# Kernel tuning notes

Hardware: AMD Instinct MI355X
Metric: run time of the kernel (lower is better)

The kernel has to match this reference:

```python
import jax, jax.numpy as jnp
import numpy as np
from jax import lax

GRID_W, GRID_H = 4, 4
N_NODES = GRID_W * GRID_H  # 16
N_NEIGH = 8
N_CLS = 10
BN_EPS = 1e-5


def _neighbors(i, w, h, mode=8):
    # exact port of Brain.neighbors (ordering matters for the concat)
    size = w * h
    out = []
    if i - w >= 0:
        out.append(i - w)
    if i % w != 0:
        out.append(i - 1)
    if (i + 1) % w != 0:
        out.append(i + 1)
    if i + w < size:
        out.append(i + w)
    if mode == 8:
        if i - w - 1 >= 0 and i % w != 0:
            out.append(i - w - 1)
        if i - w + 1 >= 0 and (i + 1) % w != 0:
            out.append(i - w + 1)
        if i + w - 1 < size and i % w != 0:
            out.append(i + w - 1)
        if i + w + 1 < size and (i + 1) % w != 0:
            out.append(i + w + 1)
    return out


def _neighbor_table():
    idx = np.full((N_NODES, N_NEIGH), 0, dtype=np.int32)
    mask = np.zeros((N_NODES, N_NEIGH), dtype=np.float32)
    for i in range(N_NODES):
        n = _neighbors(i, GRID_W, GRID_H, 8)
        idx[i, :len(n)] = np.array(n, dtype=np.int32)
        mask[i, :len(n)] = 1.0
    return jnp.asarray(idx), jnp.asarray(mask)


def _conv(x, w, b):
    y = lax.conv_general_dilated(x, w, (1, 1), 'SAME',
                                 dimension_numbers=('NCHW', 'OIHW', 'NCHW'))
    return y + b[None, :, None, None]


def _bn_train(x, g, b):
    # BatchNorm2d in training mode (module default): batch statistics
    mean = jnp.mean(x, axis=(0, 2, 3), keepdims=True)
    var = jnp.var(x, axis=(0, 2, 3), keepdims=True)
    xn = (x - mean) * lax.rsqrt(var + BN_EPS)
    return xn * g[None, :, None, None] + b[None, :, None, None]


def _maxpool(x):
    # MaxPool2d(kernel=3, stride=2, padding=1)
    return lax.reduce_window(x, -jnp.inf, lax.max,
                             (1, 1, 3, 3), (1, 1, 2, 2),
                             ((0, 0), (0, 0), (1, 1), (1, 1)))


def setup_inputs() -> dict:
    key = jax.random.key(0)
    ks = jax.random.split(key, 24)
    B = 128
    f32 = jnp.float32

    def rn(k, shape, scale):
        return jax.random.normal(k, shape, dtype=f32) * scale

    inp = {
        'x': rn(ks[0], (B, 3, 64, 64), 1.0),
        'cw1': rn(ks[1], (64, 3, 3, 3), 0.1), 'cb1': jnp.zeros((64,), f32),
        'bn1_g': jnp.ones((64,), f32), 'bn1_b': jnp.zeros((64,), f32),
        'cw2': rn(ks[2], (128, 64, 3, 3), 0.05), 'cb2': jnp.zeros((128,), f32),
        'bn2_g': jnp.ones((128,), f32), 'bn2_b': jnp.zeros((128,), f32),
        'cw3': rn(ks[3], (256, 128, 3, 3), 0.03), 'cb3': jnp.zeros((256,), f32),
        'cw4': rn(ks[4], (256, 256, 3, 3), 0.02), 'cb4': jnp.zeros((256,), f32),
        'cw5': rn(ks[5], (512, 256, 3, 3), 0.02), 'cb5': jnp.zeros((512,), f32),
        'cw6': rn(ks[6], (512, 512, 3, 3), 0.015), 'cb6': jnp.zeros((512,), f32),
        'cw7': rn(ks[7], (512, 512, 3, 3), 0.015), 'cb7': jnp.zeros((512,), f32),
        'W1': rn(ks[8], (N_NODES, 592, 600), 0.04), 'b1': jnp.zeros((N_NODES, 600), f32),
        'W2': rn(ks[9], (N_NODES, 600, N_CLS), 0.04), 'b2': jnp.zeros((N_NODES, N_CLS), f32),
    }
    return inp


def _backbone(x, cw1, cb1, bn1_g, bn1_b, cw2, cb2, bn2_g, bn2_b,
              cw3, cb3, cw4, cb4, cw5, cb5, cw6, cb6, cw7, cb7):
    h = _maxpool(jax.nn.relu(_bn_train(_conv(x, cw1, cb1), bn1_g, bn1_b)))
    h = _maxpool(jax.nn.relu(_bn_train(_conv(h, cw2, cb2), bn2_g, bn2_b)))
    h = jax.nn.relu(_conv(h, cw3, cb3))
    h = _maxpool(jax.nn.relu(_conv(h, cw4, cb4)))
    h = jax.nn.relu(_conv(h, cw5, cb5))
    h = _maxpool(jax.nn.relu(_conv(h, cw6, cb6)))
    h = jax.nn.relu(_conv(h, cw7, cb7))
    return h  # [B, 512, 4, 4]


def _colons(X, W1, b1, W2, b2):
    # X: [16, B, 592] -> softmax probs [16, B, 10]; per-node MLP
    h = jnp.tanh(jnp.einsum('nbi,nio->nbo', X, W1) + b1[:, None, :])
    logits = jnp.einsum('nbh,nho->nbo', h, W2) + b2[:, None, :]
    return jax.nn.softmax(logits, axis=-1)


def reference(x, cw1, cb1, bn1_g, bn1_b, cw2, cb2, bn2_g, bn2_b,
              cw3, cb3, cw4, cb4, cw5, cb5, cw6, cb6, cw7, cb7,
              W1, b1, W2, b2):
    B = x.shape[0]
    conv = _backbone(x, cw1, cb1, bn1_g, bn1_b, cw2, cb2, bn2_g, bn2_b,
                     cw3, cb3, cw4, cb4, cw5, cb5, cw6, cb6, cw7, cb7)
    conv = conv.reshape(B, 512, N_NODES)           # torch.flatten(conv, 2)
    feats = jnp.transpose(conv, (2, 0, 1))         # [16, B, 512]

    # first pass: neighbor slots are all-zero p1..p8
    zeros80 = jnp.zeros((N_NODES, B, N_NEIGH * N_CLS), dtype=x.dtype)
    preds1 = _colons(jnp.concatenate([zeros80, feats], axis=-1), W1, b1, W2, b2)

    # second pass: gather neighbor predictions (zero-padded to 8 slots)
    idx, mask = _neighbor_table()                  # [16,8] int, [16,8] float
    gathered = preds1[idx]                         # [16, 8, B, 10]
    gathered = gathered * mask[:, :, None, None]
    neigh = jnp.transpose(gathered, (0, 2, 1, 3)).reshape(N_NODES, B, N_NEIGH * N_CLS)
    preds2 = _colons(jnp.concatenate([neigh, feats], axis=-1), W1, b1, W2, b2)  # [16, B, 10]

    sum_preds = jnp.mean(preds2, axis=0)           # [B, 10]
    squared_sum_preds = sum_preds * sum_preds
    return squared_sum_preds, preds2
```

## Files before the change

### kernel.cpp

```cpp
#include <hip/hip_runtime.h>
#include <math.h>


#define BN_EPS 1e-5f

typedef _Float16 f16x8 __attribute__((ext_vector_type(8)));
typedef _Float16 f16x4 __attribute__((ext_vector_type(4)));
typedef float    f32x4v __attribute__((ext_vector_type(4)));

constexpr int ilog2c(int x) { return x <= 1 ? 0 : 1 + ilog2c(x >> 1); }

__device__ __forceinline__ void lds_barrier() {
    asm volatile("s_waitcnt lgkmcnt(0)\n\ts_barrier" ::: "memory");
}

__global__ __launch_bounds__(256)
void wsplit_kernel(const float* __restrict__ w, _Float16* __restrict__ o, int COCI)
{
    const int t = blockIdx.x * 256 + threadIdx.x;
    if (t >= COCI) return;
#pragma unroll
    for (int ph = 0; ph < 9; ++ph)
        o[ph * COCI + t] = (_Float16)w[t * 9 + ph];
}

__global__ void wsplit1_kernel(const float* __restrict__ w, _Float16* __restrict__ o)
{
    const int co = threadIdx.x;
#pragma unroll
    for (int k = 0; k < 32; ++k)
        o[co * 32 + k] = (k < 27) ? (_Float16)w[co * 27 + k] : (_Float16)0.f;
}

__global__ __launch_bounds__(256)
void w1t_kernel(const float* __restrict__ W1, _Float16* __restrict__ Tf,
                _Float16* __restrict__ Tn)
{
    __shared__ float T[64][65];
    const int n  = blockIdx.z;
    const int o0 = blockIdx.y * 64;
    const int k0 = blockIdx.x * 64;
    const int tid = threadIdx.x;
    const int c  = tid & 63;
    const int r4 = tid >> 6;
    const float* Wn = W1 + (size_t)n * 592 * 600;
#pragma unroll
    for (int rep = 0; rep < 16; ++rep) {
        const int kr = rep * 4 + r4;
        const int k = k0 + kr, o = o0 + c;
        float v = 0.f;
        if (k < 592 && o < 600) v = Wn[k * 600 + o];
        T[kr][c] = v;
    }
    __syncthreads();
#pragma unroll
    for (int rep = 0; rep < 16; ++rep) {
        const int orr = rep * 4 + r4;
        const int o = o0 + orr;
        const int k = k0 + c;
        const float v = T[c][orr];
        if (k >= 80 && k < 592)
            Tf[((size_t)(n * 640 + o)) * 512 + (k - 80)] = (_Float16)v;
        if (k < 96)
            Tn[((size_t)(n * 640 + o)) * 96 + k] = (k < 80) ? (_Float16)v : (_Float16)0.f;
    }
}

__global__ void b1pad_kernel(const float* __restrict__ b1, float* __restrict__ b1p)
{
    const int t = blockIdx.x * 256 + threadIdx.x;
    if (t >= 16 * 640) return;
    const int n = t / 640, o = t - n * 640;
    b1p[t] = (o < 600) ? b1[n * 600 + o] : 0.f;
}

__global__ __launch_bounds__(256)
void conv1_mfma_kernel(const float* __restrict__ in, const _Float16* __restrict__ w32,
                       _Float16* __restrict__ out, int B)
{
    __shared__ __align__(16) _Float16 As[64 * 32];
    __shared__ __align__(16) _Float16 Bs[128 * 32];

    const int tid  = threadIdx.x;
    const int pix0 = blockIdx.x * 128;
    const int bn   = tid & 127;
    const int bh   = tid >> 7;
    const int gp   = pix0 + bn;
    const int pb   = gp >> 12;
    const int sp   = gp & 4095;
    const int py   = sp >> 6;
    const int px   = sp & 63;
    const float* inb = in + (size_t)pb * 3 * 4096;

    _Float16 vals[16];
    if (bh == 0) {
#pragma unroll
        for (int u = 0; u < 16; ++u) {
            const int k = u;
            const int ci = k / 9, r = k - ci * 9, ky = r / 3, kx = r - ky * 3;
            const int iy = py + ky - 1, ix = px + kx - 1;
            float v = 0.f;
            if ((unsigned)iy < 64u && (unsigned)ix < 64u)
                v = inb[ci * 4096 + iy * 64 + ix];
            vals[u] = (_Float16)v;
        }
    } else {
#pragma unroll
        for (int u = 0; u < 16; ++u) {
            const int k = 16 + u;
            float v = 0.f;
            if (k < 27) {
                const int ci = k / 9, r = k - ci * 9, ky = r / 3, kx = r - ky * 3;
                const int iy = py + ky - 1, ix = px + kx - 1;
                if ((unsigned)iy < 64u && (unsigned)ix < 64u)
                    v = inb[ci * 4096 + iy * 64 + ix];
            }
            vals[u] = (_Float16)v;
        }
    }
    f16x8 b0, b1;
#pragma unroll
    for (int j = 0; j < 8; ++j) { b0[j] = vals[j]; b1[j] = vals[8 + j]; }
    *(f16x8*)&Bs[bn * 32 + (((2 * bh    ) ^ (bn & 3)) << 3)] = b0;
    *(f16x8*)&Bs[bn * 32 + (((2 * bh + 1) ^ (bn & 3)) << 3)] = b1;

    if (tid < 128) {
        const int arow = tid >> 1, ah = tid & 1;
        const f16x8 a0 = *(const f16x8*)(w32 + arow * 32 + ah * 16);
        const f16x8 a1 = *(const f16x8*)(w32 + arow * 32 + ah * 16 + 8);
        *(f16x8*)&As[arow * 32 + (((2 * ah    ) ^ (arow & 3)) << 3)] = a0;
        *(f16x8*)&As[arow * 32 + (((2 * ah + 1) ^ (arow & 3)) << 3)] = a1;
    }
    __syncthreads();

    const int lane = tid & 63, wv = tid >> 6;
    const int q = lane >> 4, lm = lane & 15;
    const int swz = (q ^ (lm & 3)) << 3;

    f16x8 af[4], bf[2];
#pragma unroll
    for (int ti = 0; ti < 4; ++ti)
        af[ti] = *(const f16x8*)&As[(ti * 16 + lm) * 32 + swz];
#pragma unroll
    for (int tj = 0; tj < 2; ++tj)
        bf[tj] = *(const f16x8*)&Bs[(wv * 32 + tj * 16 + lm) * 32 + swz];

    f32x4v acc[4][2];
#pragma unroll
    for (int ti = 0; ti < 4; ++ti)
#pragma unroll
        for (int tj = 0; tj < 2; ++tj)
            acc[ti][tj] = __builtin_amdgcn_mfma_f32_16x16x32_f16(
                af[ti], bf[tj], (f32x4v)0.f, 0, 0, 0);

#pragma unroll
    for (int tj = 0; tj < 2; ++tj) {
        const int gpix = pix0 + wv * 32 + tj * 16 + lm;
#pragma unroll
        for (int ti = 0; ti < 4; ++ti) {
            const int cob = ti * 16 + q * 4;
            f16x4 h4;
#pragma unroll
            for (int r = 0; r < 4; ++r) h4[r] = (_Float16)acc[ti][tj][r];
            *(f16x4*)&out[(size_t)gpix * 64 + cob] = h4;
        }
    }
}

template <int CI, int CO, int H, int W, int KSPLIT, int EPI>
__global__ __launch_bounds__(256)
void conv_pl_kernel(const _Float16* __restrict__ in, const _Float16* __restrict__ w9,
                    const float* __restrict__ bias, _Float16* __restrict__ out,
                    float* __restrict__ part, const _Float16* __restrict__ zbuf, int B)
{
    constexpr int HW   = H * W;
    constexpr int lgHW = ilog2c(HW);
    constexpr int lgW  = ilog2c(W);

    __shared__ __align__(16) _Float16 As[2][128 * 32];

    const int tid  = threadIdx.x;
    const int pix0 = blockIdx.x * 128;
    const int co0  = blockIdx.y * 128;

    const int lane = tid & 63, wv = tid >> 6;
    const int wm = (wv & 1) * 64, wn = (wv >> 1) * 64;
    const int q = lane >> 4, lm = lane & 15;
    const int swz = (q ^ (lm & 3)) << 3;

    const int arow = tid >> 1, ah = tid & 1;
    const int aw0 = ((2 * ah    ) ^ (arow & 3)) << 3;
    const int aw1 = ((2 * ah + 1) ^ (arow & 3)) << 3;
    const _Float16* abase = w9 + ((size_t)(co0 + arow)) * CI + ah * 16;

    int pbq[4], pyq[4], pxq[4];
#pragma unroll
    for (int tj = 0; tj < 4; ++tj) {
        const int gp = pix0 + wn + tj * 16 + lm;
        pbq[tj] = gp >> lgHW;
        const int sp = gp & (HW - 1);
        pyq[tj] = sp >> lgW;
        pxq[tj] = sp & (W - 1);
    }

    constexpr int CS_TOT = CI / 32;
    constexpr int CS_PER = CS_TOT / KSPLIT;
    constexpr int NIT    = 9 * CS_PER;
    const int cs0 = (KSPLIT > 1) ? blockIdx.z * CS_PER : 0;

    const _Float16* bp[4];
    auto setB = [&](int phx) {
        const int dy = phx / 3 - 1;
        const int dx = phx - (phx / 3) * 3 - 1;
#pragma unroll
        for (int tj = 0; tj < 4; ++tj) {
            const int y2 = pyq[tj] + dy, x2 = pxq[tj] + dx;
            const bool valid = ((unsigned)y2 < (unsigned)H) && ((unsigned)x2 < (unsigned)W);
            const int sp2 = (y2 << lgW) | x2;
            bp[tj] = valid ? (in + ((size_t)((pbq[tj] << lgHW) | sp2)) * CI + q * 8)
                           : (zbuf + q * 8);
        }
    };

    f32x4v acc[4][4];
#pragma unroll
    for (int i = 0; i < 4; ++i)
#pragma unroll
        for (int j = 0; j < 4; ++j) acc[i][j] = (f32x4v)0.f;

    setB(0);
    f16x8 bcur[4];
#pragma unroll
    for (int tj = 0; tj < 4; ++tj)
        bcur[tj] = *(const f16x8*)(bp[tj] + (size_t)cs0 * 32);
    {
        const f16x8 a0 = *(const f16x8*)(abase + (size_t)cs0 * 32);
        const f16x8 a1 = *(const f16x8*)(abase + (size_t)cs0 * 32 + 8);
        *(f16x8*)&As[0][arow * 32 + aw0] = a0;
        *(f16x8*)&As[0][arow * 32 + aw1] = a1;
    }

    int buf = 0, ph = 0, cs = 0;
    for (int it = 0; it < NIT; ++it) {
        int phn = ph, csn = cs + 1;
        const bool adv = (csn == CS_PER);
        if (adv) { csn = 0; phn = ph + 1; }
        const bool havenext = (it + 1 < NIT);
        f16x8 bnext[4], aN0, aN1;
        if (havenext) {
            if (adv) setB(phn);
#pragma unroll
            for (int tj = 0; tj < 4; ++tj)
                bnext[tj] = *(const f16x8*)(bp[tj] + (size_t)(cs0 + csn) * 32);
            const _Float16* aphn = abase + (size_t)phn * CO * CI;
            aN0 = *(const f16x8*)(aphn + (size_t)(cs0 + csn) * 32);
            aN1 = *(const f16x8*)(aphn + (size_t)(cs0 + csn) * 32 + 8);
        }

        lds_barrier();

        f16x8 afr[4];
#pragma unroll
        for (int ti = 0; ti < 4; ++ti)
            afr[ti] = *(const f16x8*)&As[buf][(wm + ti * 16 + lm) * 32 + swz];
#pragma unroll
        for (int ti = 0; ti < 4; ++ti)
#pragma unroll
            for (int tj = 0; tj < 4; ++tj)
                acc[ti][tj] = __builtin_amdgcn_mfma_f32_16x16x32_f16(
                    afr[ti], bcur[tj], acc[ti][tj], 0, 0, 0);

        if (havenext) {
            *(f16x8*)&As[buf ^ 1][arow * 32 + aw0] = aN0;
            *(f16x8*)&As[buf ^ 1][arow * 32 + aw1] = aN1;
            buf ^= 1;
#pragma unroll
            for (int tj = 0; tj < 4; ++tj) bcur[tj] = bnext[tj];
            ph = phn; cs = csn;
        }
    }

    if (EPI == 2) {
        float* pout = part + (size_t)blockIdx.z * ((size_t)B * HW * CO);
#pragma unroll
        for (int tj = 0; tj < 4; ++tj) {
            const int gpix = pix0 + wn + tj * 16 + lm;
#pragma unroll
            for (int ti = 0; ti < 4; ++ti) {
                const int cob = co0 + wm + ti * 16 + q * 4;
                *(float4*)&pout[(size_t)gpix * CO + cob] =
                    make_float4(acc[ti][tj][0], acc[ti][tj][1],
                                acc[ti][tj][2], acc[ti][tj][3]);
            }
        }
    } else {
#pragma unroll
        for (int tj = 0; tj < 4; ++tj) {
            const int gpix = pix0 + wn + tj * 16 + lm;
#pragma unroll
            for (int ti = 0; ti < 4; ++ti) {
                const int cob = co0 + wm + ti * 16 + q * 4;
                f16x4 h4;
                if (EPI == 1) {
                    const float4 bb4 = *(const float4*)&bias[cob];
                    h4[0] = (_Float16)fmaxf(acc[ti][tj][0] + bb4.x, 0.f);
                    h4[1] = (_Float16)fmaxf(acc[ti][tj][1] + bb4.y, 0.f);
                    h4[2] = (_Float16)fmaxf(acc[ti][tj][2] + bb4.z, 0.f);
                    h4[3] = (_Float16)fmaxf(acc[ti][tj][3] + bb4.w, 0.f);
                } else {
#pragma unroll
                    for (int r = 0; r < 4; ++r) h4[r] = (_Float16)acc[ti][tj][r];
                }
                *(f16x4*)&out[(size_t)gpix * CO + cob] = h4;
            }
        }
    }
}

template <int C>
__global__ __launch_bounds__(256)
void bn_stats_nhwc_kernel(const _Float16* __restrict__ in, float* __restrict__ sums,
                          int Ptot)
{
    constexpr int C8 = C / 8;
    constexpr int PS = 256 / C8;
    const int chunk = Ptot / gridDim.x;
    const int c8   = threadIdx.x & (C8 - 1);
    const int poff = threadIdx.x >> ilog2c(C8);
    float s[8], s2[8];
#pragma unroll
    for (int j = 0; j < 8; ++j) { s[j] = 0.f; s2[j] = 0.f; }
    const int p0 = blockIdx.x * chunk;
    for (int p = p0 + poff; p < p0 + chunk; p += PS) {
        const f16x8 v = *(const f16x8*)(in + (size_t)p * C + c8 * 8);
#pragma unroll
        for (int j = 0; j < 8; ++j) {
            const float f = (float)v[j];
            s[j] += f; s2[j] += f * f;
        }
    }
    __shared__ float ls[2 * C];
    for (int i = threadIdx.x; i < 2 * C; i += 256) ls[i] = 0.f;
    __syncthreads();
#pragma unroll
    for (int j = 0; j < 8; ++j) {
        atomicAdd(&ls[c8 * 8 + j], s[j]);
        atomicAdd(&ls[C + c8 * 8 + j], s2[j]);
    }
    __syncthreads();
    for (int i = threadIdx.x; i < 2 * C; i += 256) atomicAdd(&sums[i], ls[i]);
}

template <int C>
__global__ void bn_finalize_kernel(const float* __restrict__ sums,
                                   const float* __restrict__ g,
                                   const float* __restrict__ beta,
                                   float* __restrict__ ss, int Ntot)
{
    const int c = blockIdx.x * 64 + threadIdx.x;
    if (c >= C) return;
    const float inv   = 1.f / (float)Ntot;
    const float mean  = sums[c] * inv;
    const float var   = sums[C + c] * inv - mean * mean;
    const float scale = g[c] * rsqrtf(var + BN_EPS);
    ss[c]     = scale;
    ss[C + c] = beta[c] - mean * scale;
}

template <int C, int Hin, int Win, bool DO_BN>
__global__ __launch_bounds__(256)
void pool_nhwc_kernel(const _Float16* __restrict__ in, const float* __restrict__ ss,
                      _Float16* __restrict__ out, int B)
{
    constexpr int Ho = Hin / 2, Wo = Win / 2, C8 = C / 8;
    constexpr int lgC8 = ilog2c(C8), lgWo = ilog2c(Wo), lgHo = ilog2c(Ho);
    const int t = blockIdx.x * 256 + threadIdx.x;
    const int total = B * Ho * Wo * C8;
    if (t >= total) return;
    const int c8 = t & (C8 - 1);
    const int r1 = t >> lgC8;
    const int ox = r1 & (Wo - 1);
    const int r2 = r1 >> lgWo;
    const int oy = r2 & (Ho - 1);
    const int b  = r2 >> lgHo;

    float sc[8], sh[8];
    if (DO_BN) {
#pragma unroll
        for (int j = 0; j < 8; ++j) {
            sc[j] = ss[c8 * 8 + j];
            sh[j] = ss[C + c8 * 8 + j];
        }
    }
    float m[8];
#pragma unroll
    for (int j = 0; j < 8; ++j) m[j] = -1e30f;

    const int y0 = max(0, 2 * oy - 1), y1 = min(Hin - 1, 2 * oy + 1);
    const int x0 = max(0, 2 * ox - 1), x1 = min(Win - 1, 2 * ox + 1);
    const _Float16* ib = in + ((size_t)b * Hin * Win) * C + c8 * 8;
    for (int iy = y0; iy <= y1; ++iy)
        for (int ix = x0; ix <= x1; ++ix) {
            const f16x8 v = *(const f16x8*)(ib + (size_t)(iy * Win + ix) * C);
#pragma unroll
            for (int j = 0; j < 8; ++j) {
                float f = (float)v[j];
                if (DO_BN) f = f * sc[j] + sh[j];
                m[j] = fmaxf(m[j], f);
            }
        }
    f16x8 o;
#pragma unroll
    for (int j = 0; j < 8; ++j) {
        float f = m[j];
        if (DO_BN) f = fmaxf(f, 0.f);
        o[j] = (_Float16)f;
    }
    *(f16x8*)&out[((size_t)((b << (lgHo + lgWo)) | (oy << lgWo) | ox)) * C + c8 * 8] = o;
}

template <int CO, int Z>
__global__ __launch_bounds__(256)
void sum_bias_relu_nhwc_kernel(const float* __restrict__ part, const float* __restrict__ bias,
                               _Float16* __restrict__ out, int Npix)
{
    const int t = blockIdx.x * 256 + threadIdx.x;
    const int N8 = Npix * CO / 8;
    if (t >= N8) return;
    const size_t i8 = (size_t)t * 8;
    const int c = (int)(i8 & (CO - 1));
    const size_t S = (size_t)Npix * CO;
    float4 x0 = *(const float4*)(part + i8);
    float4 x1 = *(const float4*)(part + i8 + 4);
#pragma unroll
    for (int z = 1; z < Z; ++z) {
        const float4 p0 = *(const float4*)(part + z * S + i8);
        const float4 p1 = *(const float4*)(part + z * S + i8 + 4);
        x0.x += p0.x; x0.y += p0.y; x0.z += p0.z; x0.w += p0.w;
        x1.x += p1.x; x1.y += p1.y; x1.z += p1.z; x1.w += p1.w;
    }
    const float4 b0 = *(const float4*)(bias + c);
    const float4 b1 = *(const float4*)(bias + c + 4);
    f16x8 o;
    o[0] = (_Float16)fmaxf(x0.x + b0.x, 0.f);
    o[1] = (_Float16)fmaxf(x0.y + b0.y, 0.f);
    o[2] = (_Float16)fmaxf(x0.z + b0.z, 0.f);
    o[3] = (_Float16)fmaxf(x0.w + b0.w, 0.f);
    o[4] = (_Float16)fmaxf(x1.x + b1.x, 0.f);
    o[5] = (_Float16)fmaxf(x1.y + b1.y, 0.f);
    o[6] = (_Float16)fmaxf(x1.z + b1.z, 0.f);
    o[7] = (_Float16)fmaxf(x1.w + b1.w, 0.f);
    *(f16x8*)&out[i8] = o;
}

template <int Z>
__global__ __launch_bounds__(256)
void build_xf_kernel(const float* __restrict__ part, const float* __restrict__ bias,
                     _Float16* __restrict__ Xf, int B)
{
    const int t = blockIdx.x * 256 + threadIdx.x;
    if (t >= B * 16 * 128) return;
    const int pix = t >> 7;
    const int c   = (t & 127) * 4;
    const size_t S = (size_t)B * 16 * 512;
    float4 a = *(const float4*)(part + (size_t)pix * 512 + c);
#pragma unroll
    for (int z = 1; z < Z; ++z) {
        const float4 p = *(const float4*)(part + z * S + (size_t)pix * 512 + c);
        a.x += p.x; a.y += p.y; a.z += p.z; a.w += p.w;
    }
    const float4 bb = *(const float4*)(bias + c);
    f16x4 o4;
    o4[0] = (_Float16)fmaxf(a.x + bb.x, 0.f);
    o4[1] = (_Float16)fmaxf(a.y + bb.y, 0.f);
    o4[2] = (_Float16)fmaxf(a.z + bb.z, 0.f);
    o4[3] = (_Float16)fmaxf(a.w + bb.w, 0.f);
    const int b_ = pix >> 4, sp = pix & 15;
    *(f16x4*)&Xf[((size_t)(sp * B + b_)) * 512 + c] = o4;
}

template <int K, bool PASS2>
__global__ __launch_bounds__(256)
void fc1_mfma_kernel(const _Float16* __restrict__ Xf, const _Float16* __restrict__ W1T,
                     const float* __restrict__ b1p, float* __restrict__ pre,
                     float* __restrict__ h, int B)
{
    __shared__ __align__(16) _Float16 As[2][128 * 32];
    __shared__ __align__(16) _Float16 Bs[2][128 * 32];

    const int tid = threadIdx.x;
    const int o0  = blockIdx.x * 128;
    const int n   = blockIdx.y;

    const int lane = tid & 63, wv = tid >> 6;
    const int wm = (wv & 1) * 64, wn = (wv >> 1) * 64;
    const int q = lane >> 4, lm = lane & 15;
    const int swz = (q ^ (lm & 3)) << 3;

    const int arow = tid >> 1, ah = tid & 1;
    const int aw0 = ((2 * ah    ) ^ (arow & 3)) << 3;
    const int aw1 = ((2 * ah + 1) ^ (arow & 3)) << 3;

    const _Float16* asrc = W1T + ((size_t)(n * 640 + o0 + arow)) * K + ah * 16;
    const _Float16* bsrc = Xf  + ((size_t)(n * 128 + arow)) * K + ah * 16;

    f32x4v acc[4][4];
#pragma unroll
    for (int i = 0; i < 4; ++i)
#pragma unroll
        for (int j = 0; j < 4; ++j) acc[i][j] = (f32x4v)0.f;

    constexpr int S = K / 32;
    {
        const f16x8 a0 = *(const f16x8*)(asrc);
        const f16x8 a1 = *(const f16x8*)(asrc + 8);
        const f16x8 b0 = *(const f16x8*)(bsrc);
        const f16x8 b1 = *(const f16x8*)(bsrc + 8);
        *(f16x8*)&As[0][arow * 32 + aw0] = a0;
        *(f16x8*)&As[0][arow * 32 + aw1] = a1;
        *(f16x8*)&Bs[0][arow * 32 + aw0] = b0;
        *(f16x8*)&Bs[0][arow * 32 + aw1] = b1;
    }
    int buf = 0;
    for (int s = 0; s < S; ++s) {
        f16x8 aN0, aN1, bN0, bN1;
        if (s + 1 < S) {
            aN0 = *(const f16x8*)(asrc + (s + 1) * 32);
            aN1 = *(const f16x8*)(asrc + (s + 1) * 32 + 8);
            bN0 = *(const f16x8*)(bsrc + (s + 1) * 32);
            bN1 = *(const f16x8*)(bsrc + (s + 1) * 32 + 8);
        }
        lds_barrier();
        f16x8 afr[4], bfr[4];
#pragma unroll
        for (int ti = 0; ti < 4; ++ti)
            afr[ti] = *(const f16x8*)&As[buf][(wm + ti * 16 + lm) * 32 + swz];
#pragma unroll
        for (int tj = 0; tj < 4; ++tj)
            bfr[tj] = *(const f16x8*)&Bs[buf][(wn + tj * 16 + lm) * 32 + swz];
#pragma unroll
        for (int ti = 0; ti < 4; ++ti)
#pragma unroll
            for (int tj = 0; tj < 4; ++tj)
                acc[ti][tj] = __builtin_amdgcn_mfma_f32_16x16x32_f16(
                    afr[ti], bfr[tj], acc[ti][tj], 0, 0, 0);
        if (s + 1 < S) {
            *(f16x8*)&As[buf ^ 1][arow * 32 + aw0] = aN0;
            *(f16x8*)&As[buf ^ 1][arow * 32 + aw1] = aN1;
            *(f16x8*)&Bs[buf ^ 1][arow * 32 + aw0] = bN0;
            *(f16x8*)&Bs[buf ^ 1][arow * 32 + aw1] = bN1;
            buf ^= 1;
        }
    }

#pragma unroll
    for (int tj = 0; tj < 4; ++tj) {
        const int m = wn + tj * 16 + lm;
#pragma unroll
        for (int ti = 0; ti < 4; ++ti) {
            const int o = o0 + wm + ti * 16 + q * 4;
            const size_t oi = ((size_t)(n * 128 + m)) * 640 + o;
            float4 base;
            if (PASS2) base = *(const float4*)&pre[oi];
            else       base = *(const float4*)&b1p[n * 640 + o];
            float4 v = make_float4(acc[ti][tj][0] + base.x, acc[ti][tj][1] + base.y,
                                   acc[ti][tj][2] + base.z, acc[ti][tj][3] + base.w);
            if (!PASS2) *(float4*)&pre[oi] = v;
            *(float4*)&h[oi] = make_float4(tanhf(v.x), tanhf(v.y), tanhf(v.z), tanhf(v.w));
        }
    }
}

__global__ __launch_bounds__(128)
void colon_fc2_kernel(const float* __restrict__ h, const float* __restrict__ W2,
                      const float* __restrict__ b2, float* __restrict__ preds, int B)
{
    const int n = blockIdx.x;
    __shared__ float W2s[6000];
    __shared__ float b2s[10];
    for (int i = threadIdx.x; i < 6000; i += 128) W2s[i] = W2[n * 6000 + i];
    if (threadIdx.x < 10) b2s[threadIdx.x] = b2[n * 10 + threadIdx.x];
    __syncthreads();

    for (int b = threadIdx.x; b < B; b += 128) {
        float l[10];
#pragma unroll
        for (int c = 0; c < 10; ++c) l[c] = b2s[c];
        const float* hp = h + ((size_t)(n * B + b)) * 640;
        for (int k = 0; k < 600; k += 4) {
            const float4 hv = *reinterpret_cast<const float4*>(&hp[k]);
            const float hh[4] = {hv.x, hv.y, hv.z, hv.w};
#pragma unroll
            for (int u = 0; u < 4; ++u)
#pragma unroll
                for (int c = 0; c < 10; ++c)
                    l[c] += hh[u] * W2s[(k + u) * 10 + c];
        }
        float mx = l[0];
#pragma unroll
        for (int c = 1; c < 10; ++c) mx = fmaxf(mx, l[c]);
        float s = 0.f;
#pragma unroll
        for (int c = 0; c < 10; ++c) { l[c] = expf(l[c] - mx); s += l[c]; }
        const float inv = 1.f / s;
        float* pp = preds + ((size_t)(n * B + b)) * 10;
#pragma unroll
        for (int c = 0; c < 10; ++c) pp[c] = l[c] * inv;
    }
}

__global__ __launch_bounds__(256)
void fill_neigh_kernel(const float* __restrict__ preds1, _Float16* __restrict__ Xn, int B)
{
    const int t = blockIdx.x * 256 + threadIdx.x;
    if (t >= 16 * B * 96) return;
    const int col = t % 96;
    const int b   = (t / 96) % B;
    const int n   = t / (96 * B);

    float v = 0.f;
    if (col < 80) {
        const int j = col / 10, c = col - j * 10;
        int lst[8];
        int cnt = 0;
        const int w = 4, sz = 16, i = n;
        if (i - w >= 0)                                lst[cnt++] = i - w;
        if (i % w != 0)                                lst[cnt++] = i - 1;
        if ((i + 1) % w != 0)                          lst[cnt++] = i + 1;
        if (i + w < sz)                                lst[cnt++] = i + w;
        if (i - w - 1 >= 0 && i % w != 0)              lst[cnt++] = i - w - 1;
        if (i - w + 1 >= 0 && (i + 1) % w != 0)        lst[cnt++] = i - w + 1;
        if (i + w - 1 < sz && i % w != 0)              lst[cnt++] = i + w - 1;
        if (i + w + 1 < sz && (i + 1) % w != 0)        lst[cnt++] = i + w + 1;
        if (j < cnt) v = preds1[((size_t)(lst[j] * B + b)) * 10 + c];
    }
    Xn[t] = (_Float16)v;
}

__global__ __launch_bounds__(256)
void final_out_kernel(const float* __restrict__ preds2, float* __restrict__ out0, int B)
{
    const int t = blockIdx.x * 256 + threadIdx.x;
    if (t >= B * 10) return;
    const int b = t / 10, c = t % 10;
    float s = 0.f;
#pragma unroll
    for (int n = 0; n < 16; ++n)
        s += preds2[((size_t)(n * B + b)) * 10 + c];
    const float m = s * (1.f / 16.f);
    out0[t] = m * m;
}

extern "C" void kernel_launch(void* const* d_in, const int* in_sizes, int n_in,
                              void* d_out, int out_size, void* d_ws, size_t ws_size,
                              hipStream_t stream)
{
    const float* x    = (const float*)d_in[0];
    const float* cw1  = (const float*)d_in[1];
    const float* bn1g = (const float*)d_in[3];
    const float* bn1b = (const float*)d_in[4];
    const float* cw2  = (const float*)d_in[5];
    const float* bn2g = (const float*)d_in[7];
    const float* bn2b = (const float*)d_in[8];
    const float* cw3  = (const float*)d_in[9];
    const float* cb3  = (const float*)d_in[10];
    const float* cw4  = (const float*)d_in[11];
    const float* cb4  = (const float*)d_in[12];
    const float* cw5  = (const float*)d_in[13];
    const float* cb5  = (const float*)d_in[14];
    const float* cw6  = (const float*)d_in[15];
    const float* cb6  = (const float*)d_in[16];
    const float* cw7  = (const float*)d_in[17];
    const float* cb7  = (const float*)d_in[18];
    const float* W1   = (const float*)d_in[19];
    const float* b1   = (const float*)d_in[20];
    const float* W2   = (const float*)d_in[21];
    const float* b2   = (const float*)d_in[22];

    const int B = in_sizes[0] / (3 * 64 * 64);

    float* ws = (float*)d_ws;
    float*     P    = ws;
    _Float16*  A    = (_Float16*)(ws + 8388608);
    _Float16*  Bb   = (_Float16*)(ws + 25165824);
    _Float16*  wreg = (_Float16*)(ws + 33554432);
    _Float16*  W1Tf = (_Float16*)(ws + 36984832);
    _Float16*  W1Tn = (_Float16*)(ws + 39606272);
    _Float16*  Xf16 = (_Float16*)(ws + 40097792);
    _Float16*  Xn16 = (_Float16*)(ws + 40622080);
    float*     b1p  = ws + 40720384;
    float*     preb = ws + 40730624;
    float*     hb   = ws + 42041344;
    float*     small= ws + 43352064;
    float* sums1  = small;
    float* sums2  = small + 256;
    float* ss1    = small + 1024;
    float* ss2    = small + 1536;
    float* preds1 = small + 2048;
    _Float16* zbuf = (_Float16*)(small + 32768);

    _Float16* w1f  = wreg;
    _Float16* w9c2 = wreg + 2048;
    _Float16* w9c3 = w9c2 + 73728;
    _Float16* w9c4 = w9c3 + 294912;
    _Float16* w9c5 = w9c4 + 589824;
    _Float16* w9c6 = w9c5 + 1179648;
    _Float16* w9c7 = w9c6 + 2359296;

    float* out0   = (float*)d_out;
    float* preds2 = (float*)d_out + (size_t)B * 10;

    hipMemsetAsync(small, 0, 512 * sizeof(float), stream);
    hipMemsetAsync(zbuf, 0, 4096, stream);

    wsplit1_kernel<<<1, 64, 0, stream>>>(cw1, w1f);
    wsplit_kernel<<<(128 * 64  + 255) / 256, 256, 0, stream>>>(cw2, w9c2, 128 * 64);
    wsplit_kernel<<<(256 * 128 + 255) / 256, 256, 0, stream>>>(cw3, w9c3, 256 * 128);
    wsplit_kernel<<<(256 * 256 + 255) / 256, 256, 0, stream>>>(cw4, w9c4, 256 * 256);
    wsplit_kernel<<<(512 * 256 + 255) / 256, 256, 0, stream>>>(cw5, w9c5, 512 * 256);
    wsplit_kernel<<<(512 * 512 + 255) / 256, 256, 0, stream>>>(cw6, w9c6, 512 * 512);
    wsplit_kernel<<<(512 * 512 + 255) / 256, 256, 0, stream>>>(cw7, w9c7, 512 * 512);
    w1t_kernel<<<dim3(10, 10, 16), 256, 0, stream>>>(W1, W1Tf, W1Tn);
    b1pad_kernel<<<(16 * 640 + 255) / 256, 256, 0, stream>>>(b1, b1p);

    conv1_mfma_kernel<<<B * 4096 / 128, 256, 0, stream>>>(x, w1f, A, B);
    bn_stats_nhwc_kernel<64><<<512, 256, 0, stream>>>(A, sums1, B * 4096);
    bn_finalize_kernel<64><<<1, 64, 0, stream>>>(sums1, bn1g, bn1b, ss1, B * 4096);
    pool_nhwc_kernel<64, 64, 64, true>
        <<<(B * 1024 * 8 + 255) / 256, 256, 0, stream>>>(A, ss1, Bb, B);

    conv_pl_kernel<64, 128, 32, 32, 1, 0>
        <<<dim3(B * 1024 / 128, 1), 256, 0, stream>>>(Bb, w9c2, nullptr, A, nullptr, zbuf, B);
    bn_stats_nhwc_kernel<128><<<256, 256, 0, stream>>>(A, sums2, B * 1024);
    bn_finalize_kernel<128><<<2, 64, 0, stream>>>(sums2, bn2g, bn2b, ss2, B * 1024);
    pool_nhwc_kernel<128, 32, 32, true>
        <<<(B * 256 * 16 + 255) / 256, 256, 0, stream>>>(A, ss2, Bb, B);

    conv_pl_kernel<128, 256, 16, 16, 1, 1>
        <<<dim3(B * 256 / 128, 2), 256, 0, stream>>>(Bb, w9c3, cb3, A, nullptr, zbuf, B);
    conv_pl_kernel<256, 256, 16, 16, 1, 1>
        <<<dim3(B * 256 / 128, 2), 256, 0, stream>>>(A, w9c4, cb4, Bb, nullptr, zbuf, B);
    pool_nhwc_kernel<256, 16, 16, false>
        <<<(B * 64 * 32 + 255) / 256, 256, 0, stream>>>(Bb, nullptr, A, B);

    conv_pl_kernel<256, 512, 8, 8, 2, 2>
        <<<dim3(B * 64 / 128, 4, 2), 256, 0, stream>>>(A, w9c5, nullptr, nullptr, P, zbuf, B);
    sum_bias_relu_nhwc_kernel<512, 2>
        <<<(B * 64 * 512 / 8 + 255) / 256, 256, 0, stream>>>(P, cb5, Bb, B * 64);

    conv_pl_kernel<512, 512, 8, 8, 2, 2>
        <<<dim3(B * 64 / 128, 4, 2), 256, 0, stream>>>(Bb, w9c6, nullptr, nullptr, P, zbuf, B);
    sum_bias_relu_nhwc_kernel<512, 2>
        <<<(B * 64 * 512 / 8 + 255) / 256, 256, 0, stream>>>(P, cb6, A, B * 64);
    pool_nhwc_kernel<512, 8, 8, false>
        <<<(B * 16 * 64 + 255) / 256, 256, 0, stream>>>(A, nullptr, Bb, B);

    conv_pl_kernel<512, 512, 4, 4, 8, 2>
        <<<dim3(B * 16 / 128, 4, 8), 256, 0, stream>>>(Bb, w9c7, nullptr, nullptr, P, zbuf, B);

    build_xf_kernel<8><<<(B * 16 * 128 + 255) / 256, 256, 0, stream>>>(P, cb7, Xf16, B);

    fc1_mfma_kernel<512, false>
        <<<dim3(5, 16), 256, 0, stream>>>(Xf16, W1Tf, b1p, preb, hb, B);
    colon_fc2_kernel<<<16, 128, 0, stream>>>(hb, W2, b2, preds1, B);

    fill_neigh_kernel<<<(16 * B * 96 + 255) / 256, 256, 0, stream>>>(preds1, Xn16, B);
    fc1_mfma_kernel<96, true>
        <<<dim3(5, 16), 256, 0, stream>>>(Xn16, W1Tn, b1p, preb, hb, B);
    colon_fc2_kernel<<<16, 128, 0, stream>>>(hb, W2, b2, preds2, B);

    final_out_kernel<<<(B * 10 + 255) / 256, 256, 0, stream>>>(preds2, out0, B);
}
```

Before: 732.9 us.

## Stage B operand through LDS with triple-buffered two-deep prefetch; merge weight prep kernels

The conv implicit-GEMM kernel now loads the activation (B) tile cooperatively into LDS instead of each wave fetching its own fragments from global memory. Both A and B tiles are triple-buffered, with register prefetch running two iterations ahead, so each iteration needs only one barrier. This is meant to cut redundant global loads of B across the two M-waves and hide load latency better, at the cost of doubling LDS use, which may lower occupancy. The seven weight-split launches are also merged into a single kernel with one grid row per layer, saving launch overhead.

```diff
diff --git a/kernel.cpp b/kernel.cpp
--- a/kernel.cpp
+++ b/kernel.cpp
@@ -15,21 +15,36 @@
 }
 
 __global__ __launch_bounds__(256)
-void wsplit_kernel(const float* __restrict__ w, _Float16* __restrict__ o, int COCI)
-{
+void wprep_kernel(const float* __restrict__ cw1, const float* __restrict__ cw2,
+                  const float* __restrict__ cw3, const float* __restrict__ cw4,
+                  const float* __restrict__ cw5, const float* __restrict__ cw6,
+                  const float* __restrict__ cw7, _Float16* __restrict__ wreg)
+{
+    const int layer = blockIdx.y;
     const int t = blockIdx.x * 256 + threadIdx.x;
-    if (t >= COCI) return;
+    if (layer == 0) {
+        if (t < 64) {
+#pragma unroll
+            for (int k = 0; k < 32; ++k)
+                wreg[t * 32 + k] = (k < 27) ? (_Float16)cw1[t * 27 + k] : (_Float16)0.f;
+        }
+        return;
+    }
+    const float* src = nullptr;
+    _Float16* dst = nullptr;
+    int n = 0;
+    switch (layer) {
+        case 1: src = cw2; dst = wreg + 2048;    n = 8192;   break;
+        case 2: src = cw3; dst = wreg + 75776;   n = 32768;  break;
+        case 3: src = cw4; dst = wreg + 370688;  n = 65536;  break;
+        case 4: src = cw5; dst = wreg + 960512;  n = 131072; break;
+        case 5: src = cw6; dst = wreg + 2140160; n = 262144; break;
+        case 6: src = cw7; dst = wreg + 4499456; n = 262144; break;
+    }
+    if (t >= n) return;
 #pragma unroll
     for (int ph = 0; ph < 9; ++ph)
-        o[ph * COCI + t] = (_Float16)w[t * 9 + ph];
-}
-
-__global__ void wsplit1_kernel(const float* __restrict__ w, _Float16* __restrict__ o)
-{
-    const int co = threadIdx.x;
-#pragma unroll
-    for (int k = 0; k < 32; ++k)
-        o[co * 32 + k] = (k < 27) ? (_Float16)w[co * 27 + k] : (_Float16)0.f;
+        dst[ph * n + t] = (_Float16)src[t * 9 + ph];
 }
 
 __global__ __launch_bounds__(256)
@@ -169,7 +184,7 @@
 
 template <int CI, int CO, int H, int W, int KSPLIT, int EPI>
 __global__ __launch_bounds__(256)
-void conv_pl_kernel(const _Float16* __restrict__ in, const _Float16* __restrict__ w9,
+void conv_p2_kernel(const _Float16* __restrict__ in, const _Float16* __restrict__ w9,
                     const float* __restrict__ bias, _Float16* __restrict__ out,
                     float* __restrict__ part, const _Float16* __restrict__ zbuf, int B)
 {
@@ -177,7 +192,8 @@
     constexpr int lgHW = ilog2c(HW);
     constexpr int lgW  = ilog2c(W);
 
-    __shared__ __align__(16) _Float16 As[2][128 * 32];
+    __shared__ __align__(16) _Float16 As[3][128 * 32];
+    __shared__ __align__(16) _Float16 Bs[3][128 * 32];
 
     const int tid  = threadIdx.x;
     const int pix0 = blockIdx.x * 128;
@@ -193,33 +209,28 @@
     const int aw1 = ((2 * ah + 1) ^ (arow & 3)) << 3;
     const _Float16* abase = w9 + ((size_t)(co0 + arow)) * CI + ah * 16;
 
-    int pbq[4], pyq[4], pxq[4];
-#pragma unroll
-    for (int tj = 0; tj < 4; ++tj) {
-        const int gp = pix0 + wn + tj * 16 + lm;
-        pbq[tj] = gp >> lgHW;
-        const int sp = gp & (HW - 1);
-        pyq[tj] = sp >> lgW;
-        pxq[tj] = sp & (W - 1);
-    }
+    const int bn = tid & 127, bh = tid >> 7;
+    const int gp = pix0 + bn;
+    const int pb = gp >> lgHW;
+    const int spx = gp & (HW - 1);
+    const int py = spx >> lgW, px = spx & (W - 1);
+    const int bw0 = ((2 * bh    ) ^ (bn & 3)) << 3;
+    const int bw1 = ((2 * bh + 1) ^ (bn & 3)) << 3;
 
     constexpr int CS_TOT = CI / 32;
     constexpr int CS_PER = CS_TOT / KSPLIT;
     constexpr int NIT    = 9 * CS_PER;
     const int cs0 = (KSPLIT > 1) ? blockIdx.z * CS_PER : 0;
 
-    const _Float16* bp[4];
+    const _Float16* bstage;
     auto setB = [&](int phx) {
         const int dy = phx / 3 - 1;
         const int dx = phx - (phx / 3) * 3 - 1;
-#pragma unroll
-        for (int tj = 0; tj < 4; ++tj) {
-            const int y2 = pyq[tj] + dy, x2 = pxq[tj] + dx;
-            const bool valid = ((unsigned)y2 < (unsigned)H) && ((unsigned)x2 < (unsigned)W);
-            const int sp2 = (y2 << lgW) | x2;
-            bp[tj] = valid ? (in + ((size_t)((pbq[tj] << lgHW) | sp2)) * CI + q * 8)
-                           : (zbuf + q * 8);
-        }
+        const int y2 = py + dy, x2 = px + dx;
+        const bool valid = ((unsigned)y2 < (unsigned)H) && ((unsigned)x2 < (unsigned)W);
+        const int sp2 = (y2 << lgW) | x2;
+        bstage = valid ? (in + ((size_t)((pb << lgHW) | sp2)) * CI + bh * 16)
+                       : (zbuf + bh * 16);
     };
 
     f32x4v acc[4][4];
@@ -228,56 +239,51 @@
 #pragma unroll
         for (int j = 0; j < 4; ++j) acc[i][j] = (f32x4v)0.f;
 
+    f16x8 aq[2][2], bq[2][2];
+    int lph = 0, lcs = 0;
     setB(0);
-    f16x8 bcur[4];
-#pragma unroll
-    for (int tj = 0; tj < 4; ++tj)
-        bcur[tj] = *(const f16x8*)(bp[tj] + (size_t)cs0 * 32);
-    {
-        const f16x8 a0 = *(const f16x8*)(abase + (size_t)cs0 * 32);
-        const f16x8 a1 = *(const f16x8*)(abase + (size_t)cs0 * 32 + 8);
-        *(f16x8*)&As[0][arow * 32 + aw0] = a0;
-        *(f16x8*)&As[0][arow * 32 + aw1] = a1;
-    }
-
-    int buf = 0, ph = 0, cs = 0;
+    auto loadT = [&](int s) {
+        const _Float16* ap = abase + (size_t)lph * CO * CI + (size_t)(cs0 + lcs) * 32;
+        aq[s][0] = *(const f16x8*)ap;
+        aq[s][1] = *(const f16x8*)(ap + 8);
+        const _Float16* bp2 = bstage + (size_t)(cs0 + lcs) * 32;
+        bq[s][0] = *(const f16x8*)bp2;
+        bq[s][1] = *(const f16x8*)(bp2 + 8);
+        if (++lcs == CS_PER) { lcs = 0; ++lph; if (lph < 9) setB(lph); }
+    };
+    loadT(0);
+    loadT(1);
+    *(f16x8*)&As[0][arow * 32 + aw0] = aq[0][0];
+    *(f16x8*)&As[0][arow * 32 + aw1] = aq[0][1];
+    *(f16x8*)&Bs[0][bn * 32 + bw0]   = bq[0][0];
+    *(f16x8*)&Bs[0][bn * 32 + bw1]   = bq[0][1];
+
+#pragma unroll 6
     for (int it = 0; it < NIT; ++it) {
-        int phn = ph, csn = cs + 1;
-        const bool adv = (csn == CS_PER);
-        if (adv) { csn = 0; phn = ph + 1; }
-        const bool havenext = (it + 1 < NIT);
-        f16x8 bnext[4], aN0, aN1;
-        if (havenext) {
-            if (adv) setB(phn);
-#pragma unroll
-            for (int tj = 0; tj < 4; ++tj)
-                bnext[tj] = *(const f16x8*)(bp[tj] + (size_t)(cs0 + csn) * 32);
-            const _Float16* aphn = abase + (size_t)phn * CO * CI;
-            aN0 = *(const f16x8*)(aphn + (size_t)(cs0 + csn) * 32);
-            aN1 = *(const f16x8*)(aphn + (size_t)(cs0 + csn) * 32 + 8);
-        }
-
+        if (it + 2 < NIT) loadT(it & 1);
+        if (it + 1 < NIT) {
+            const int s1 = (it + 1) & 1;
+            const int wb = (it + 1) % 3;
+            *(f16x8*)&As[wb][arow * 32 + aw0] = aq[s1][0];
+            *(f16x8*)&As[wb][arow * 32 + aw1] = aq[s1][1];
+            *(f16x8*)&Bs[wb][bn * 32 + bw0]   = bq[s1][0];
+            *(f16x8*)&Bs[wb][bn * 32 + bw1]   = bq[s1][1];
+        }
         lds_barrier();
-
-        f16x8 afr[4];
+        const int rb = it % 3;
+        f16x8 afr[4], bfr[4];
 #pragma unroll
         for (int ti = 0; ti < 4; ++ti)
-            afr[ti] = *(const f16x8*)&As[buf][(wm + ti * 16 + lm) * 32 + swz];
+            afr[ti] = *(const f16x8*)&As[rb][(wm + ti * 16 + lm) * 32 + swz];
+#pragma unroll
+        for (int tj = 0; tj < 4; ++tj)
+            bfr[tj] = *(const f16x8*)&Bs[rb][(wn + tj * 16 + lm) * 32 + swz];
 #pragma unroll
         for (int ti = 0; ti < 4; ++ti)
 #pragma unroll
             for (int tj = 0; tj < 4; ++tj)
                 acc[ti][tj] = __builtin_amdgcn_mfma_f32_16x16x32_f16(
-                    afr[ti], bcur[tj], acc[ti][tj], 0, 0, 0);
-
-        if (havenext) {
-            *(f16x8*)&As[buf ^ 1][arow * 32 + aw0] = aN0;
-            *(f16x8*)&As[buf ^ 1][arow * 32 + aw1] = aN1;
-            buf ^= 1;
-#pragma unroll
-            for (int tj = 0; tj < 4; ++tj) bcur[tj] = bnext[tj];
-            ph = phn; cs = csn;
-        }
+                    afr[ti], bfr[tj], acc[ti][tj], 0, 0, 0);
     }
 
     if (EPI == 2) {
@@ -699,29 +705,23 @@
     float* preds1 = small + 2048;
     _Float16* zbuf = (_Float16*)(small + 32768);
 
+    float* out0   = (float*)d_out;
+    float* preds2 = (float*)d_out + (size_t)B * 10;
+
+    hipMemsetAsync(small, 0, 512 * sizeof(float), stream);
+    hipMemsetAsync(zbuf, 0, 4096, stream);
+
+    wprep_kernel<<<dim3(1024, 7), 256, 0, stream>>>(cw1, cw2, cw3, cw4, cw5, cw6, cw7, wreg);
+    w1t_kernel<<<dim3(10, 10, 16), 256, 0, stream>>>(W1, W1Tf, W1Tn);
+    b1pad_kernel<<<(16 * 640 + 255) / 256, 256, 0, stream>>>(b1, b1p);
+
     _Float16* w1f  = wreg;
     _Float16* w9c2 = wreg + 2048;
-    _Float16* w9c3 = w9c2 + 73728;
-    _Float16* w9c4 = w9c3 + 294912;
-    _Float16* w9c5 = w9c4 + 589824;
-    _Float16* w9c6 = w9c5 + 1179648;
-    _Float16* w9c7 = w9c6 + 2359296;
-
-    float* out0   = (float*)d_out;
-    float* preds2 = (float*)d_out + (size_t)B * 10;
-
-    hipMemsetAsync(small, 0, 512 * sizeof(float), stream);
-    hipMemsetAsync(zbuf, 0, 4096, stream);
-
-    wsplit1_kernel<<<1, 64, 0, stream>>>(cw1, w1f);
-    wsplit_kernel<<<(128 * 64  + 255) / 256, 256, 0, stream>>>(cw2, w9c2, 128 * 64);
-    wsplit_kernel<<<(256 * 128 + 255) / 256, 256, 0, stream>>>(cw3, w9c3, 256 * 128);
-    wsplit_kernel<<<(256 * 256 + 255) / 256, 256, 0, stream>>>(cw4, w9c4, 256 * 256);
-    wsplit_kernel<<<(512 * 256 + 255) / 256, 256, 0, stream>>>(cw5, w9c5, 512 * 256);
-    wsplit_kernel<<<(512 * 512 + 255) / 256, 256, 0, stream>>>(cw6, w9c6, 512 * 512);
-    wsplit_kernel<<<(512 * 512 + 255) / 256, 256, 0, stream>>>(cw7, w9c7, 512 * 512);
-    w1t_kernel<<<dim3(10, 10, 16), 256, 0, stream>>>(W1, W1Tf, W1Tn);
-    b1pad_kernel<<<(16 * 640 + 255) / 256, 256, 0, stream>>>(b1, b1p);
+    _Float16* w9c3 = wreg + 75776;
+    _Float16* w9c4 = wreg + 370688;
+    _Float16* w9c5 = wreg + 960512;
+    _Float16* w9c6 = wreg + 2140160;
+    _Float16* w9c7 = wreg + 4499456;
 
     conv1_mfma_kernel<<<B * 4096 / 128, 256, 0, stream>>>(x, w1f, A, B);
     bn_stats_nhwc_kernel<64><<<512, 256, 0, stream>>>(A, sums1, B * 4096);
@@ -729,33 +729,33 @@
     pool_nhwc_kernel<64, 64, 64, true>
         <<<(B * 1024 * 8 + 255) / 256, 256, 0, stream>>>(A, ss1, Bb, B);
 
-    conv_pl_kernel<64, 128, 32, 32, 1, 0>
+    conv_p2_kernel<64, 128, 32, 32, 1, 0>
         <<<dim3(B * 1024 / 128, 1), 256, 0, stream>>>(Bb, w9c2, nullptr, A, nullptr, zbuf, B);
     bn_stats_nhwc_kernel<128><<<256, 256, 0, stream>>>(A, sums2, B * 1024);
     bn_finalize_kernel<128><<<2, 64, 0, stream>>>(sums2, bn2g, bn2b, ss2, B * 1024);
     pool_nhwc_kernel<128, 32, 32, true>
         <<<(B * 256 * 16 + 255) / 256, 256, 0, stream>>>(A, ss2, Bb, B);
 
-    conv_pl_kernel<128, 256, 16, 16, 1, 1>
+    conv_p2_kernel<128, 256, 16, 16, 1, 1>
         <<<dim3(B * 256 / 128, 2), 256, 0, stream>>>(Bb, w9c3, cb3, A, nullptr, zbuf, B);
-    conv_pl_kernel<256, 256, 16, 16, 1, 1>
+    conv_p2_kernel<256, 256, 16, 16, 1, 1>
         <<<dim3(B * 256 / 128, 2), 256, 0, stream>>>(A, w9c4, cb4, Bb, nullptr, zbuf, B);
     pool_nhwc_kernel<256, 16, 16, false>
         <<<(B * 64 * 32 + 255) / 256, 256, 0, stream>>>(Bb, nullptr, A, B);
 
-    conv_pl_kernel<256, 512, 8, 8, 2, 2>
+    conv_p2_kernel<256, 512, 8, 8, 2, 2>
         <<<dim3(B * 64 / 128, 4, 2), 256, 0, stream>>>(A, w9c5, nullptr, nullptr, P, zbuf, B);
     sum_bias_relu_nhwc_kernel<512, 2>
         <<<(B * 64 * 512 / 8 + 255) / 256, 256, 0, stream>>>(P, cb5, Bb, B * 64);
 
-    conv_pl_kernel<512, 512, 8, 8, 2, 2>
+    conv_p2_kernel<512, 512, 8, 8, 2, 2>
         <<<dim3(B * 64 / 128, 4, 2), 256, 0, stream>>>(Bb, w9c6, nullptr, nullptr, P, zbuf, B);
     sum_bias_relu_nhwc_kernel<512, 2>
         <<<(B * 64 * 512 / 8 + 255) / 256, 256, 0, stream>>>(P, cb6, A, B * 64);
     pool_nhwc_kernel<512, 8, 8, false>
         <<<(B * 16 * 64 + 255) / 256, 256, 0, stream>>>(A, nullptr, Bb, B);
 
-    conv_pl_kernel<512, 512, 4, 4, 8, 2>
+    conv_p2_kernel<512, 512, 4, 4, 8, 2>
         <<<dim3(B * 16 / 128, 4, 8), 256, 0, stream>>>(Bb, w9c7, nullptr, nullptr, P, zbuf, B);
 
     build_xf_kernel<8><<<(B * 16 * 128 + 255) / 256, 256, 0, stream>>>(P, cb7, Xf16, B);
```

After: 633.9 us. 1.16x faster.
